# Optimization experiments

Measured on AMD Instinct MI355X. Metric: run time of the kernel, lower is better.

The kernel has to match this reference:

```python
import jax, jax.numpy as jnp
import numpy as np

IN_F = 128
OUT_F = 64


def _xavier(key, shape, gain=1.414):
    fan_in, fan_out = shape[0], shape[1]
    bound = gain * np.sqrt(6.0 / (fan_in + fan_out))
    return jax.random.uniform(key, shape, jnp.float32, -bound, bound)


def setup_inputs() -> dict:
    key = jax.random.key(0)
    ks = jax.random.split(key, 11)
    features = jax.random.normal(ks[0], (2, 32, 2048, IN_F), dtype=jnp.float32)
    d = {"features": features}
    for i in range(4):
        d[f"W{i+1}"] = _xavier(ks[1 + 2 * i], (IN_F, 2 * OUT_F))
        d[f"a{i+1}"] = _xavier(ks[2 + 2 * i], (2 * OUT_F, 1))
    d["Wo"] = _xavier(ks[9], (8 * OUT_F, OUT_F))
    return d


def _head(features, W, a):
    # features: [b,g,n,i]; W: [i,j]; a: [j,1]
    Wx = jnp.einsum('bgni,ij->bgnj', features, W)          # [b,g,n,2F]
    att = jax.nn.softmax(Wx @ a, axis=2)                   # softmax over nodes, [b,g,n,1]
    return jnp.einsum('bgno,bgnj->bgj', att, Wx)           # pooled [b,g,2F]


def reference(features, W1, a1, W2, a2, W3, a3, W4, a4, Wo):
    h1 = _head(features, W1, a1)
    h2 = _head(features, W2, a2)
    h3 = _head(features, W3, a3)
    h4 = _head(features, W4, a4)
    multi = jnp.concatenate([h1, h2, h3, h4], axis=2)      # [b,g,8F]
    return jax.nn.elu(multi @ Wo)                          # [b,g,F]
```

## Files before the change

### kernel.cpp

```cpp
#include <hip/hip_runtime.h>
#include <math.h>

#define BG     64
#define NN     2048
#define F      128
#define OUTF   64
#define NSLICE 64
#define SNODES 32

#define OFF_WEFF 0
#define OFF_FP   512
#define OFF_LP   (512 + BG * NSLICE * 4 * F)

__global__ __launch_bounds__(256) void k_weff(
    const float* __restrict__ W1, const float* __restrict__ a1,
    const float* __restrict__ W2, const float* __restrict__ a2,
    const float* __restrict__ W3, const float* __restrict__ a3,
    const float* __restrict__ W4, const float* __restrict__ a4,
    float* __restrict__ ws) {
  int h = blockIdx.x, t = threadIdx.x;
  const float* W = (h == 0) ? W1 : (h == 1) ? W2 : (h == 2) ? W3 : W4;
  const float* a = (h == 0) ? a1 : (h == 1) ? a2 : (h == 2) ? a3 : a4;
  __shared__ float aL[F];
  __shared__ float part[F][33];

  if (t < F) aL[t] = a[t];
  __syncthreads();

  int c = t & 31, r8 = t >> 5;
#pragma unroll
  for (int it = 0; it < 16; ++it) {
    int row = it * 8 + r8;
    float4 w = ((const float4*)(W + row * F))[c];
    part[row][c] = w.x * aL[4 * c] + w.y * aL[4 * c + 1] +
                   w.z * aL[4 * c + 2] + w.w * aL[4 * c + 3];
  }
  __syncthreads();

  if (t < F) {
    float s = 0.f;
#pragma unroll
    for (int c2 = 0; c2 < 32; ++c2) s += part[t][c2];
    ws[OFF_WEFF + h * F + t] = s;
  }
}

__global__ __launch_bounds__(256) void k_main(
    const float* __restrict__ feat, float* __restrict__ ws) {
  int g = blockIdx.x >> 6;
  int slice = blockIdx.x & (NSLICE - 1);
  int t = threadIdx.x;

  __shared__ float4 sfeat[SNODES * 32];
  __shared__ float4 weffL[4 * 32];
  __shared__ float eLf[SNODES * 4];
  __shared__ float4 pacc[4][2][32];
  __shared__ float sePf[2][4];

  if (t < 128) weffL[t] = ((const float4*)(ws + OFF_WEFF))[t];

  const float4* fb =
      (const float4*)(feat + ((size_t)g * NN + slice * SNODES) * F);
  float4 ld[4];
#pragma unroll
  for (int k = 0; k < 4; ++k) ld[k] = fb[k * 256 + t];
#pragma unroll
  for (int k = 0; k < 4; ++k) {
    int j = k * 256 + t;
    int n = j >> 5, c = j & 31;
    sfeat[n * 32 + (c ^ n)] = ld[k];
  }
  __syncthreads();

  if (t < 128) {
    int n = t & 31, h = t >> 5;
    int base = n * 32, wb = h * 32;
    float p = 0.f;
#pragma unroll 8
    for (int c = 0; c < 32; ++c) {
      float4 f = sfeat[base + (c ^ n)];
      float4 w = weffL[wb + c];
      p += f.x * w.x + f.y * w.y + f.z * w.z + f.w * w.w;
    }
    eLf[n * 4 + h] = __expf(p);
  }
  __syncthreads();

  {
    int i4 = t & 31, q = (t >> 5) & 1, h = t >> 6;
    float4 a0 = make_float4(0.f, 0.f, 0.f, 0.f);
    float se = 0.f;
#pragma unroll 8
    for (int nn = 0; nn < 16; ++nn) {
      int n = q * 16 + nn;
      float4 f = sfeat[n * 32 + (i4 ^ n)];
      float e = eLf[n * 4 + h];
      a0.x += e * f.x; a0.y += e * f.y; a0.z += e * f.z; a0.w += e * f.w;
      se += e;
    }
    pacc[h][q][i4] = a0;
    if (i4 == 0) sePf[q][h] = se;
  }
  __syncthreads();

  if (t < 128) {
    int i4 = t & 31, h = t >> 5;
    float4 s0 = pacc[h][0][i4], s1 = pacc[h][1][i4];
    float4 s = make_float4(s0.x + s1.x, s0.y + s1.y,
                           s0.z + s1.z, s0.w + s1.w);
    ((float4*)(ws + OFF_FP))[(size_t)(g * NSLICE + slice) * 128 + h * 32 + i4] = s;
  }
  if (t == 0) {
    float4 L = make_float4(sePf[0][0] + sePf[1][0], sePf[0][1] + sePf[1][1],
                           sePf[0][2] + sePf[1][2], sePf[0][3] + sePf[1][3]);
    ((float4*)(ws + OFF_LP))[g * NSLICE + slice] = L;
  }
}

__global__ __launch_bounds__(256) void k_final(
    const float* __restrict__ W1, const float* __restrict__ W2,
    const float* __restrict__ W3, const float* __restrict__ W4,
    const float* __restrict__ Wo, const float* __restrict__ ws,
    float* __restrict__ out) {
  int g = blockIdx.x;
  int t = threadIdx.x;

  __shared__ float4 f4[896];
  __shared__ float invl[4];
  float* fbuf = (float*)f4;

  const float4* FP4 = (const float4*)(ws + OFF_FP) + (size_t)g * NSLICE * 128;

  if (t < 4) {
    float s = 0.f;
#pragma unroll
    for (int sl = 0; sl < NSLICE; ++sl)
      s += ws[OFF_LP + (g * NSLICE + sl) * 4 + t];
    invl[t] = 1.0f / s;
  }
  {
    int j = t & 127, half = t >> 7;
    float4 s4 = make_float4(0.f, 0.f, 0.f, 0.f);
#pragma unroll
    for (int sl = 0; sl < 32; ++sl) {
      float4 v = FP4[(size_t)(half * 32 + sl) * 128 + j];
      s4.x += v.x; s4.y += v.y; s4.z += v.z; s4.w += v.w;
    }
    f4[half * 128 + j] = s4;
  }
  __syncthreads();
  if (t < 128) {
    float4 a = f4[t], b = f4[128 + t];
    float inv = invl[t >> 5];
    f4[256 + t] = make_float4((a.x + b.x) * inv, (a.y + b.y) * inv,
                              (a.z + b.z) * inv, (a.w + b.w) * inv);
  }
  __syncthreads();

  {
    int c = t & 31, rg = (t >> 5) & 1, h = t >> 6;
    const float* Wsel = (h == 0) ? W1 : (h == 1) ? W2 : (h == 2) ? W3 : W4;
    const float4* W4p = (const float4*)Wsel;
    const float* fph = fbuf + 1024 + h * F;
    float4 acc = make_float4(0.f, 0.f, 0.f, 0.f);
#pragma unroll 8
    for (int k = 0; k < 64; ++k) {
      int i = rg * 64 + k;
      float s = fph[i];
      float4 w = W4p[i * 32 + c];
      acc.x += s * w.x; acc.y += s * w.y; acc.z += s * w.z; acc.w += s * w.w;
    }
    f4[512 + (h * 2 + rg) * 32 + c] = acc;
  }
  __syncthreads();
  if (t < 128) {
    int h = t >> 5, c = t & 31;
    float4 a = f4[512 + (h * 2) * 32 + c];
    float4 b = f4[512 + (h * 2 + 1) * 32 + c];
    f4[768 + h * 32 + c] = make_float4(a.x + b.x, a.y + b.y,
                                       a.z + b.z, a.w + b.w);
  }
  __syncthreads();

  {
    int o4 = t & 15, rg = t >> 4;
    const float4* Wo4 = (const float4*)Wo;
    const float* mu = fbuf + 3072;
    float4 acc = make_float4(0.f, 0.f, 0.f, 0.f);
#pragma unroll 8
    for (int k = 0; k < 32; ++k) {
      int i = rg * 32 + k;
      float s = mu[i];
      float4 w = Wo4[i * 16 + o4];
      acc.x += s * w.x; acc.y += s * w.y; acc.z += s * w.z; acc.w += s * w.w;
    }
    f4[rg * 16 + o4] = acc;
  }
  __syncthreads();
  if (t < OUTF) {
    float s = 0.f;
#pragma unroll
    for (int rg = 0; rg < 16; ++rg) s += fbuf[rg * 64 + t];
    out[g * OUTF + t] = (s > 0.f) ? s : expm1f(s);
  }
}

extern "C" void kernel_launch(void* const* d_in, const int* in_sizes, int n_in,
                              void* d_out, int out_size, void* d_ws, size_t ws_size,
                              hipStream_t stream) {
  const float* feat = (const float*)d_in[0];
  const float* W1 = (const float*)d_in[1];
  const float* a1 = (const float*)d_in[2];
  const float* W2 = (const float*)d_in[3];
  const float* a2 = (const float*)d_in[4];
  const float* W3 = (const float*)d_in[5];
  const float* a3 = (const float*)d_in[6];
  const float* W4 = (const float*)d_in[7];
  const float* a4 = (const float*)d_in[8];
  const float* Wo = (const float*)d_in[9];
  float* ws = (float*)d_ws;
  float* out = (float*)d_out;

  k_weff<<<4, 256, 0, stream>>>(W1, a1, W2, a2, W3, a3, W4, a4, ws);
  k_main<<<BG * NSLICE, 256, 0, stream>>>(feat, ws);
  k_final<<<BG, 256, 0, stream>>>(W1, W2, W3, W4, Wo, ws, out);
}
```

Before: 121.5 us.

## Compute attention logits in registers with DPP row reductions over larger node slices

The main kernel no longer stages features in shared memory. Each thread keeps 8 feature columns of several nodes in registers, computes per-head logits with partial dot products, and reduces them across 16 lanes with DPP adds. It then accumulates exp-weighted features directly, and a single shared-memory reduction combines rows at the end. Each block now covers 128 nodes instead of 32, giving fewer blocks and smaller partial buffers for the final kernel to sum, at the cost of more registers per thread and less parallelism.

Result: slower. 125.1 us (+3.0%).

```diff
diff --git a/kernel.cpp b/kernel.cpp
--- a/kernel.cpp
+++ b/kernel.cpp
@@ -5,12 +5,29 @@
 #define NN     2048
 #define F      128
 #define OUTF   64
-#define NSLICE 64
-#define SNODES 32
+#define NSLICE 16
+#define SNODES 128
 
 #define OFF_WEFF 0
 #define OFF_FP   512
 #define OFF_LP   (512 + BG * NSLICE * 4 * F)
+
+template <int CTRL>
+__device__ __forceinline__ float dpp_add(float x) {
+  int y = __builtin_amdgcn_update_dpp(0, __float_as_int(x), CTRL, 0xF, 0xF, true);
+  return x + __int_as_float(y);
+}
+__device__ __forceinline__ float rowsum16(float x) {
+  x = dpp_add<0x121>(x);
+  x = dpp_add<0x122>(x);
+  x = dpp_add<0x124>(x);
+  x = dpp_add<0x128>(x);
+  return x;
+}
+__device__ __forceinline__ float dot8(float4 a0, float4 a1, float4 b0, float4 b1) {
+  return a0.x * b0.x + a0.y * b0.y + a0.z * b0.z + a0.w * b0.w +
+         a1.x * b1.x + a1.y * b1.y + a1.z * b1.z + a1.w * b1.w;
+}
 
 __global__ __launch_bounds__(256) void k_weff(
     const float* __restrict__ W1, const float* __restrict__ a1,
@@ -47,72 +64,88 @@
 
 __global__ __launch_bounds__(256) void k_main(
     const float* __restrict__ feat, float* __restrict__ ws) {
-  int g = blockIdx.x >> 6;
+  int g = blockIdx.x >> 4;
   int slice = blockIdx.x & (NSLICE - 1);
   int t = threadIdx.x;
-
-  __shared__ float4 sfeat[SNODES * 32];
-  __shared__ float4 weffL[4 * 32];
-  __shared__ float eLf[SNODES * 4];
-  __shared__ float4 pacc[4][2][32];
-  __shared__ float sePf[2][4];
-
-  if (t < 128) weffL[t] = ((const float4*)(ws + OFF_WEFF))[t];
+  int r = t >> 4;
+  int c8 = t & 15;
+
+  const float4* wp = (const float4*)(ws + OFF_WEFF);
+  float4 w4[4][2];
+#pragma unroll
+  for (int h = 0; h < 4; ++h) {
+    w4[h][0] = wp[h * 32 + c8 * 2 + 0];
+    w4[h][1] = wp[h * 32 + c8 * 2 + 1];
+  }
 
   const float4* fb =
       (const float4*)(feat + ((size_t)g * NN + slice * SNODES) * F);
-  float4 ld[4];
-#pragma unroll
-  for (int k = 0; k < 4; ++k) ld[k] = fb[k * 256 + t];
-#pragma unroll
-  for (int k = 0; k < 4; ++k) {
-    int j = k * 256 + t;
-    int n = j >> 5, c = j & 31;
-    sfeat[n * 32 + (c ^ n)] = ld[k];
-  }
+
+  float4 acc[4][2];
+#pragma unroll
+  for (int h = 0; h < 4; ++h) {
+    acc[h][0] = make_float4(0.f, 0.f, 0.f, 0.f);
+    acc[h][1] = make_float4(0.f, 0.f, 0.f, 0.f);
+  }
+  float4 se = make_float4(0.f, 0.f, 0.f, 0.f);
+
+#pragma unroll
+  for (int kk = 0; kk < 2; ++kk) {
+    float4 ld[4][2];
+#pragma unroll
+    for (int b = 0; b < 4; ++b) {
+      int nl = (kk * 4 + b) * 16 + r;
+      ld[b][0] = fb[nl * 32 + c8 * 2 + 0];
+      ld[b][1] = fb[nl * 32 + c8 * 2 + 1];
+    }
+#pragma unroll
+    for (int b = 0; b < 4; ++b) {
+      float px = dot8(ld[b][0], ld[b][1], w4[0][0], w4[0][1]);
+      float py = dot8(ld[b][0], ld[b][1], w4[1][0], w4[1][1]);
+      float pz = dot8(ld[b][0], ld[b][1], w4[2][0], w4[2][1]);
+      float pw = dot8(ld[b][0], ld[b][1], w4[3][0], w4[3][1]);
+      px = rowsum16(px); py = rowsum16(py);
+      pz = rowsum16(pz); pw = rowsum16(pw);
+      float4 e = make_float4(__expf(px), __expf(py), __expf(pz), __expf(pw));
+      se.x += e.x; se.y += e.y; se.z += e.z; se.w += e.w;
+#pragma unroll
+      for (int h = 0; h < 4; ++h) {
+        float eh = (h == 0) ? e.x : (h == 1) ? e.y : (h == 2) ? e.z : e.w;
+        acc[h][0].x += eh * ld[b][0].x; acc[h][0].y += eh * ld[b][0].y;
+        acc[h][0].z += eh * ld[b][0].z; acc[h][0].w += eh * ld[b][0].w;
+        acc[h][1].x += eh * ld[b][1].x; acc[h][1].y += eh * ld[b][1].y;
+        acc[h][1].z += eh * ld[b][1].z; acc[h][1].w += eh * ld[b][1].w;
+      }
+    }
+  }
+
+  __shared__ float4 red[4][16][33];
+  __shared__ float4 seR[16];
+#pragma unroll
+  for (int h = 0; h < 4; ++h) {
+    red[h][r][c8 * 2 + 0] = acc[h][0];
+    red[h][r][c8 * 2 + 1] = acc[h][1];
+  }
+  if (c8 == 0) seR[r] = se;
   __syncthreads();
 
   if (t < 128) {
-    int n = t & 31, h = t >> 5;
-    int base = n * 32, wb = h * 32;
-    float p = 0.f;
-#pragma unroll 8
-    for (int c = 0; c < 32; ++c) {
-      float4 f = sfeat[base + (c ^ n)];
-      float4 w = weffL[wb + c];
-      p += f.x * w.x + f.y * w.y + f.z * w.z + f.w * w.w;
-    }
-    eLf[n * 4 + h] = __expf(p);
-  }
-  __syncthreads();
-
-  {
-    int i4 = t & 31, q = (t >> 5) & 1, h = t >> 6;
-    float4 a0 = make_float4(0.f, 0.f, 0.f, 0.f);
-    float se = 0.f;
-#pragma unroll 8
-    for (int nn = 0; nn < 16; ++nn) {
-      int n = q * 16 + nn;
-      float4 f = sfeat[n * 32 + (i4 ^ n)];
-      float e = eLf[n * 4 + h];
-      a0.x += e * f.x; a0.y += e * f.y; a0.z += e * f.z; a0.w += e * f.w;
-      se += e;
-    }
-    pacc[h][q][i4] = a0;
-    if (i4 == 0) sePf[q][h] = se;
-  }
-  __syncthreads();
-
-  if (t < 128) {
-    int i4 = t & 31, h = t >> 5;
-    float4 s0 = pacc[h][0][i4], s1 = pacc[h][1][i4];
-    float4 s = make_float4(s0.x + s1.x, s0.y + s1.y,
-                           s0.z + s1.z, s0.w + s1.w);
-    ((float4*)(ws + OFF_FP))[(size_t)(g * NSLICE + slice) * 128 + h * 32 + i4] = s;
+    int h = t >> 5, c4 = t & 31;
+    float4 s = make_float4(0.f, 0.f, 0.f, 0.f);
+#pragma unroll
+    for (int rr = 0; rr < 16; ++rr) {
+      float4 v = red[h][rr][c4];
+      s.x += v.x; s.y += v.y; s.z += v.z; s.w += v.w;
+    }
+    ((float4*)(ws + OFF_FP))[(size_t)(g * NSLICE + slice) * 128 + h * 32 + c4] = s;
   }
   if (t == 0) {
-    float4 L = make_float4(sePf[0][0] + sePf[1][0], sePf[0][1] + sePf[1][1],
-                           sePf[0][2] + sePf[1][2], sePf[0][3] + sePf[1][3]);
+    float4 L = make_float4(0.f, 0.f, 0.f, 0.f);
+#pragma unroll
+    for (int rr = 0; rr < 16; ++rr) {
+      float4 v = seR[rr];
+      L.x += v.x; L.y += v.y; L.z += v.z; L.w += v.w;
+    }
     ((float4*)(ws + OFF_LP))[g * NSLICE + slice] = L;
   }
 }
@@ -142,8 +175,8 @@
     int j = t & 127, half = t >> 7;
     float4 s4 = make_float4(0.f, 0.f, 0.f, 0.f);
 #pragma unroll
-    for (int sl = 0; sl < 32; ++sl) {
-      float4 v = FP4[(size_t)(half * 32 + sl) * 128 + j];
+    for (int sl = 0; sl < 8; ++sl) {
+      float4 v = FP4[(size_t)(half * 8 + sl) * 128 + j];
       s4.x += v.x; s4.y += v.y; s4.z += v.z; s4.w += v.w;
     }
     f4[half * 128 + j] = s4;
```
